# Optimization experiments

Hardware: AMD Instinct MI355X
Metric: run time of the kernel (lower is better)

## Reference

```python
import jax, jax.numpy as jnp
import numpy as np

B, T, L = 512, 512, 128  # batch, seq_len, tag-vocab size (incl. START=126, STOP=127)


def setup_inputs() -> dict:
    key = jax.random.key(0)
    k1, k2, k3 = jax.random.split(key, 3)
    # scale emissions so exp(gold path score) stays finite in fp32
    feats = jax.random.normal(k1, (B, T, L), dtype=jnp.float32) * 0.05
    # xavier_normal on [L, L] -> std = sqrt(2/(L+L)) = 1/sqrt(L)
    transfer = jax.random.normal(k2, (L, L), dtype=jnp.float32) * (1.0 / np.sqrt(L))
    target = jax.random.randint(k3, (B, T), 0, L - 2, dtype=jnp.int32)
    return {"feats": feats, "transfer": transfer, "target": target,
            "start": L - 2, "stop": L - 1}


def _crf_loss(feats, transfer, target, start, stop):
    # feats: [B, T, L] emissions; transfer: [L, L]; target: [B, T] gold tags
    Bb, Tt, Ll = feats.shape

    # ---- forward algorithm (log-sum-exp DP over tags) ----
    # scores[1] = feats[1] + transfer[start, :]
    prev0 = feats[:, 1] + transfer[start][None, :]  # [B, L]

    def step(prev, f_t):
        # original: scores[t, y] = LSE_x( scores[t-1, x] + feats[t, x] + transfer[x, y] )
        v = prev + f_t                                        # [B, L] over prev-tag x
        new = jax.nn.logsumexp(v[:, :, None] + transfer[None, :, :], axis=1)  # [B, L]
        return new, None

    step = jax.checkpoint(step)  # keep scan residuals to just the carries
    feats_rest = jnp.swapaxes(feats[:, 2:], 0, 1)  # [T-2, B, L]
    prev, _ = jax.lax.scan(step, prev0, feats_rest)
    sentence_score = jax.nn.logsumexp(prev + transfer[:, stop][None, :], axis=1)  # [B]

    # ---- gold path score ----
    emit0 = feats[:, 0, start]  # hh[0, start]
    emit = jnp.take_along_axis(feats[:, 1:], target[:, 1:, None], axis=2)[..., 0].sum(axis=1)
    pre = jnp.concatenate(
        [jnp.full((Bb, 1), start, dtype=target.dtype), target[:, 1:Tt - 1]], axis=1)  # [B, T-1]
    # original reads transfer[pre, tgt].data[0] -> detached constant
    trans = jax.lax.stop_gradient(transfer[pre, target[:, 1:]]).sum(axis=1)
    gold_score = jnp.exp(emit0 + emit + trans)  # original returns torch.exp(score)

    return sentence_score - gold_score  # per-sentence loss, shape [B]


def reference(feats, transfer, target, start, stop):
    return _crf_loss(feats, transfer, target, start, stop)
```

## Files before the change

kernel.cpp:

```cpp
#include <hip/hip_runtime.h>
#include <hip/hip_bf16.h>

#define T_DIM 512
#define L_DIM 128

typedef _Float16 h2 __attribute__((ext_vector_type(2)));

#if defined(__has_builtin)
#if __has_builtin(__builtin_amdgcn_fdot2)
#define HAS_FDOT2 1
#endif
#endif

__device__ __forceinline__ float fdot2_acc(h2 a, h2 b, float c) {
#ifdef HAS_FDOT2
    return __builtin_amdgcn_fdot2(a, b, c, false);
#else
    return c + (float)a.x * (float)b.x + (float)a.y * (float)b.y;
#endif
}

__device__ __forceinline__ h2 pack_f16(float a, float b) {
    return __builtin_bit_cast(h2, __builtin_amdgcn_cvt_pkrtz(a, b));
}

__device__ __forceinline__ void lds_barrier() {
    asm volatile("s_waitcnt lgkmcnt(0)\n\ts_barrier" ::: "memory");
}

__global__ __launch_bounds__(512, 4) void crf_fwd_kernel(
    const float* __restrict__ feats,
    const float* __restrict__ transfer,
    const int* __restrict__ target,
    const int* __restrict__ startp,
    const int* __restrict__ stopp,
    float* __restrict__ out)
{
    __shared__ unsigned short LdsU[2][L_DIM] __attribute__((aligned(16)));
    __shared__ float LdsRed[32];

    const int tid  = threadIdx.x;
    const int lane = tid & 63;
    const int wv   = tid >> 6;
    const int jj   = lane & 15;
    const int iq   = lane >> 4;
    const int j    = (wv << 4) | jj;
    const int i0   = iq << 5;
    const int b    = blockIdx.x;
    const int start = startp[0];
    const int stop  = stopp[0];
    const float* fbase = feats + (size_t)b * T_DIM * L_DIM;
    const float LOG128 = 4.852030263919617f;

    h2 Ecol[16];
#pragma unroll
    for (int q = 0; q < 16; ++q) {
        float e0 = __expf(transfer[(i0 + 2 * q)     * L_DIM + j]) * 0.0078125f;
        float e1 = __expf(transfer[(i0 + 2 * q + 1) * L_DIM + j]) * 0.0078125f;
        Ecol[q] = pack_f16(e0, e1);
    }
    const float trStop = transfer[j * L_DIM + stop];

    {
        float v2 = fbase[1 * L_DIM + j] + fbase[2 * L_DIM + j]
                 + transfer[start * L_DIM + j];
        if (iq == 0) {
            _Float16 h = (_Float16)__expf(v2);
            LdsU[0][j] = __builtin_bit_cast(unsigned short, h);
        }
    }
    float fa = fbase[3 * L_DIM + j];
    float fb = fbase[4 * L_DIM + j];
    float S  = 0.f;
    lds_barrier();

    int cur = 0;
    float accFinal = 0.f;

    for (int t = 2; t <= T_DIM - 1; ++t) {
        int tp = t + 3; if (tp > T_DIM - 1) tp = T_DIM - 1;
        float fnew = fbase[tp * L_DIM + j];
        float fexp = __expf(fa);

        if ((t & 15) == 0) {
            _Float16 h0 = __builtin_bit_cast(_Float16, LdsU[cur][0]);
            float u0 = (float)h0;
            fexp *= 1.0f / u0;
            S += __logf(u0);
        }

        const uint4* P4 = reinterpret_cast<const uint4*>(&LdsU[cur][0]);
        uint4 pa = P4[(iq << 2) | 0];
        uint4 pb = P4[(iq << 2) | 1];
        uint4 pc = P4[(iq << 2) | 2];
        uint4 pd = P4[(iq << 2) | 3];

        float a0 = 0.f, a1 = 0.f, a2 = 0.f, a3 = 0.f;
        a0 = fdot2_acc(__builtin_bit_cast(h2, pa.x), Ecol[0],  a0);
        a0 = fdot2_acc(__builtin_bit_cast(h2, pa.y), Ecol[1],  a0);
        a0 = fdot2_acc(__builtin_bit_cast(h2, pa.z), Ecol[2],  a0);
        a0 = fdot2_acc(__builtin_bit_cast(h2, pa.w), Ecol[3],  a0);
        a1 = fdot2_acc(__builtin_bit_cast(h2, pb.x), Ecol[4],  a1);
        a1 = fdot2_acc(__builtin_bit_cast(h2, pb.y), Ecol[5],  a1);
        a1 = fdot2_acc(__builtin_bit_cast(h2, pb.z), Ecol[6],  a1);
        a1 = fdot2_acc(__builtin_bit_cast(h2, pb.w), Ecol[7],  a1);
        a2 = fdot2_acc(__builtin_bit_cast(h2, pc.x), Ecol[8],  a2);
        a2 = fdot2_acc(__builtin_bit_cast(h2, pc.y), Ecol[9],  a2);
        a2 = fdot2_acc(__builtin_bit_cast(h2, pc.z), Ecol[10], a2);
        a2 = fdot2_acc(__builtin_bit_cast(h2, pc.w), Ecol[11], a2);
        a3 = fdot2_acc(__builtin_bit_cast(h2, pd.x), Ecol[12], a3);
        a3 = fdot2_acc(__builtin_bit_cast(h2, pd.y), Ecol[13], a3);
        a3 = fdot2_acc(__builtin_bit_cast(h2, pd.z), Ecol[14], a3);
        a3 = fdot2_acc(__builtin_bit_cast(h2, pd.w), Ecol[15], a3);
        float acc = (a0 + a1) + (a2 + a3);

        acc += __shfl_xor(acc, 16);
        acc += __shfl_xor(acc, 32);

        if (t < T_DIM - 1) {
            float un = acc * fexp;
            fa = fb; fb = fnew;
            if (iq == 0) {
                _Float16 h = (_Float16)un;
                LdsU[cur ^ 1][j] = __builtin_bit_cast(unsigned short, h);
            }
            lds_barrier();
            cur ^= 1;
        } else {
            accFinal = acc;
        }
    }

    S += 510.0f * LOG128;

    float x  = __logf(accFinal) + S + trStop;
    float mx = x;
#pragma unroll
    for (int d = 1; d < 64; d <<= 1) mx = fmaxf(mx, __shfl_xor(mx, d));
    float ex = (iq == 0) ? __expf(x - mx) : 0.f;
#pragma unroll
    for (int d = 1; d < 64; d <<= 1) ex += __shfl_xor(ex, d);
    if (lane == 0) { LdsRed[wv] = mx; LdsRed[8 + wv] = ex; }

    float es = 0.f, ts = 0.f;
    {
        int t = 1 + tid;
        if (t < T_DIM) {
            int tg = target[b * T_DIM + t];
            es = fbase[t * L_DIM + tg];
            int pr = (t == 1) ? start : target[b * T_DIM + t - 1];
            ts = transfer[pr * L_DIM + tg];
        }
    }
#pragma unroll
    for (int d = 1; d < 64; d <<= 1) {
        es += __shfl_xor(es, d);
        ts += __shfl_xor(ts, d);
    }
    if (lane == 0) { LdsRed[16 + wv] = es; LdsRed[24 + wv] = ts; }
    __syncthreads();

    if (tid == 0) {
        float M = LdsRed[0];
#pragma unroll
        for (int k = 1; k < 8; ++k) M = fmaxf(M, LdsRed[k]);
        float Ssum = 0.f;
#pragma unroll
        for (int k = 0; k < 8; ++k) Ssum += LdsRed[8 + k] * __expf(LdsRed[k] - M);
        float sentence = M + __logf(Ssum);
        float em = 0.f, tn = 0.f;
#pragma unroll
        for (int k = 0; k < 8; ++k) { em += LdsRed[16 + k]; tn += LdsRed[24 + k]; }
        float emit0 = fbase[start];
        out[b] = sentence - __expf(emit0 + em + tn);
    }
}

extern "C" void kernel_launch(void* const* d_in, const int* in_sizes, int n_in,
                              void* d_out, int out_size, void* d_ws, size_t ws_size,
                              hipStream_t stream) {
    const float* feats    = (const float*)d_in[0];
    const float* transfer = (const float*)d_in[1];
    const int*   target   = (const int*)d_in[2];
    const int*   startp   = (const int*)d_in[3];
    const int*   stopp    = (const int*)d_in[4];
    float* outp = (float*)d_out;
    int B = in_sizes[0] / (T_DIM * L_DIM);
    hipLaunchKernelGGL(crf_fwd_kernel, dim3(B), dim3(512), 0, stream,
                       feats, transfer, target, startp, stopp, outp);
}
```

Measured before the change: 396.3 us.

## Run each sequence's CRF recursion on a single wavefront without barriers

```diff
diff --git a/kernel.cpp b/kernel.cpp
--- a/kernel.cpp
+++ b/kernel.cpp
@@ -24,11 +24,11 @@
     return __builtin_bit_cast(h2, __builtin_amdgcn_cvt_pkrtz(a, b));
 }
 
-__device__ __forceinline__ void lds_barrier() {
-    asm volatile("s_waitcnt lgkmcnt(0)\n\ts_barrier" ::: "memory");
+__device__ __forceinline__ h2 uint_as_h2(unsigned int v) {
+    return __builtin_bit_cast(h2, v);
 }
 
-__global__ __launch_bounds__(512, 4) void crf_fwd_kernel(
+__global__ __launch_bounds__(64, 1) void crf_fwd_kernel(
     const float* __restrict__ feats,
     const float* __restrict__ transfer,
     const int* __restrict__ target,
@@ -36,120 +36,119 @@
     const int* __restrict__ stopp,
     float* __restrict__ out)
 {
-    __shared__ unsigned short LdsU[2][L_DIM] __attribute__((aligned(16)));
-    __shared__ float LdsRed[32];
+    __shared__ unsigned int LdsU[2][64] __attribute__((aligned(16)));
 
-    const int tid  = threadIdx.x;
-    const int lane = tid & 63;
-    const int wv   = tid >> 6;
-    const int jj   = lane & 15;
-    const int iq   = lane >> 4;
-    const int j    = (wv << 4) | jj;
-    const int i0   = iq << 5;
+    const int lane = threadIdx.x;
+    const int p    = lane;
+    const int j0   = p << 1;
+    const int j1   = j0 | 1;
     const int b    = blockIdx.x;
     const int start = startp[0];
     const int stop  = stopp[0];
     const float* fbase = feats + (size_t)b * T_DIM * L_DIM;
+    const float2* f2 = reinterpret_cast<const float2*>(fbase);
     const float LOG128 = 4.852030263919617f;
 
-    h2 Ecol[16];
+    h2 E0[64], E1[64];
 #pragma unroll
-    for (int q = 0; q < 16; ++q) {
-        float e0 = __expf(transfer[(i0 + 2 * q)     * L_DIM + j]) * 0.0078125f;
-        float e1 = __expf(transfer[(i0 + 2 * q + 1) * L_DIM + j]) * 0.0078125f;
-        Ecol[q] = pack_f16(e0, e1);
+    for (int q = 0; q < 64; ++q) {
+        const float2* r0 = reinterpret_cast<const float2*>(transfer + (2 * q) * L_DIM + j0);
+        const float2* r1 = reinterpret_cast<const float2*>(transfer + (2 * q + 1) * L_DIM + j0);
+        float2 e0 = *r0;
+        float2 e1 = *r1;
+        E0[q] = pack_f16(__expf(e0.x) * 0.0078125f, __expf(e1.x) * 0.0078125f);
+        E1[q] = pack_f16(__expf(e0.y) * 0.0078125f, __expf(e1.y) * 0.0078125f);
     }
-    const float trStop = transfer[j * L_DIM + stop];
+    const float trS0 = transfer[j0 * L_DIM + stop];
+    const float trS1 = transfer[j1 * L_DIM + stop];
 
     {
-        float v2 = fbase[1 * L_DIM + j] + fbase[2 * L_DIM + j]
-                 + transfer[start * L_DIM + j];
-        if (iq == 0) {
-            _Float16 h = (_Float16)__expf(v2);
-            LdsU[0][j] = __builtin_bit_cast(unsigned short, h);
-        }
+        float2 f1v = f2[1 * 64 + p];
+        float2 f2v = f2[2 * 64 + p];
+        const float2* ts = reinterpret_cast<const float2*>(transfer + start * L_DIM + j0);
+        float2 tsv = *ts;
+        float v0 = f1v.x + f2v.x + tsv.x;
+        float v1 = f1v.y + f2v.y + tsv.y;
+        LdsU[0][p] = __builtin_bit_cast(unsigned int, pack_f16(__expf(v0), __expf(v1)));
     }
-    float fa = fbase[3 * L_DIM + j];
-    float fb = fbase[4 * L_DIM + j];
-    float S  = 0.f;
-    lds_barrier();
+    float2 fa = f2[3 * 64 + p];
+    float2 fb = f2[4 * 64 + p];
+    float S = 0.f;
 
     int cur = 0;
-    float accFinal = 0.f;
+    float accF0 = 0.f, accF1 = 0.f;
 
     for (int t = 2; t <= T_DIM - 1; ++t) {
         int tp = t + 3; if (tp > T_DIM - 1) tp = T_DIM - 1;
-        float fnew = fbase[tp * L_DIM + j];
-        float fexp = __expf(fa);
+        float2 fnew = f2[tp * 64 + p];
+        float fe0 = __expf(fa.x);
+        float fe1 = __expf(fa.y);
+
+        asm volatile("s_waitcnt lgkmcnt(0)" ::: "memory");
+        const uint4* P4 = reinterpret_cast<const uint4*>(&LdsU[cur][0]);
+        uint4 R[16];
+#pragma unroll
+        for (int r = 0; r < 16; ++r) R[r] = P4[r];
 
         if ((t & 15) == 0) {
-            _Float16 h0 = __builtin_bit_cast(_Float16, LdsU[cur][0]);
-            float u0 = (float)h0;
-            fexp *= 1.0f / u0;
+            float u0 = (float)uint_as_h2(R[0].x).x;
+            float rr = __builtin_amdgcn_rcpf(u0);
             S += __logf(u0);
+            fe0 *= rr; fe1 *= rr;
         }
 
-        const uint4* P4 = reinterpret_cast<const uint4*>(&LdsU[cur][0]);
-        uint4 pa = P4[(iq << 2) | 0];
-        uint4 pb = P4[(iq << 2) | 1];
-        uint4 pc = P4[(iq << 2) | 2];
-        uint4 pd = P4[(iq << 2) | 3];
-
         float a0 = 0.f, a1 = 0.f, a2 = 0.f, a3 = 0.f;
-        a0 = fdot2_acc(__builtin_bit_cast(h2, pa.x), Ecol[0],  a0);
-        a0 = fdot2_acc(__builtin_bit_cast(h2, pa.y), Ecol[1],  a0);
-        a0 = fdot2_acc(__builtin_bit_cast(h2, pa.z), Ecol[2],  a0);
-        a0 = fdot2_acc(__builtin_bit_cast(h2, pa.w), Ecol[3],  a0);
-        a1 = fdot2_acc(__builtin_bit_cast(h2, pb.x), Ecol[4],  a1);
-        a1 = fdot2_acc(__builtin_bit_cast(h2, pb.y), Ecol[5],  a1);
-        a1 = fdot2_acc(__builtin_bit_cast(h2, pb.z), Ecol[6],  a1);
-        a1 = fdot2_acc(__builtin_bit_cast(h2, pb.w), Ecol[7],  a1);
-        a2 = fdot2_acc(__builtin_bit_cast(h2, pc.x), Ecol[8],  a2);
-        a2 = fdot2_acc(__builtin_bit_cast(h2, pc.y), Ecol[9],  a2);
-        a2 = fdot2_acc(__builtin_bit_cast(h2, pc.z), Ecol[10], a2);
-        a2 = fdot2_acc(__builtin_bit_cast(h2, pc.w), Ecol[11], a2);
-        a3 = fdot2_acc(__builtin_bit_cast(h2, pd.x), Ecol[12], a3);
-        a3 = fdot2_acc(__builtin_bit_cast(h2, pd.y), Ecol[13], a3);
-        a3 = fdot2_acc(__builtin_bit_cast(h2, pd.z), Ecol[14], a3);
-        a3 = fdot2_acc(__builtin_bit_cast(h2, pd.w), Ecol[15], a3);
-        float acc = (a0 + a1) + (a2 + a3);
-
-        acc += __shfl_xor(acc, 16);
-        acc += __shfl_xor(acc, 32);
+        float c0 = 0.f, c1 = 0.f, c2 = 0.f, c3 = 0.f;
+#pragma unroll
+        for (int r = 0; r < 16; ++r) {
+            h2 u0p = uint_as_h2(R[r].x);
+            h2 u1p = uint_as_h2(R[r].y);
+            h2 u2p = uint_as_h2(R[r].z);
+            h2 u3p = uint_as_h2(R[r].w);
+            a0 = fdot2_acc(u0p, E0[4 * r + 0], a0);
+            a1 = fdot2_acc(u1p, E0[4 * r + 1], a1);
+            a2 = fdot2_acc(u2p, E0[4 * r + 2], a2);
+            a3 = fdot2_acc(u3p, E0[4 * r + 3], a3);
+            c0 = fdot2_acc(u0p, E1[4 * r + 0], c0);
+            c1 = fdot2_acc(u1p, E1[4 * r + 1], c1);
+            c2 = fdot2_acc(u2p, E1[4 * r + 2], c2);
+            c3 = fdot2_acc(u3p, E1[4 * r + 3], c3);
+        }
+        float acc0 = (a0 + a1) + (a2 + a3);
+        float acc1 = (c0 + c1) + (c2 + c3);
 
         if (t < T_DIM - 1) {
-            float un = acc * fexp;
+            float un0 = acc0 * fe0;
+            float un1 = acc1 * fe1;
             fa = fb; fb = fnew;
-            if (iq == 0) {
-                _Float16 h = (_Float16)un;
-                LdsU[cur ^ 1][j] = __builtin_bit_cast(unsigned short, h);
-            }
-            lds_barrier();
+            LdsU[cur ^ 1][p] = __builtin_bit_cast(unsigned int, pack_f16(un0, un1));
             cur ^= 1;
         } else {
-            accFinal = acc;
+            accF0 = acc0; accF1 = acc1;
         }
     }
 
     S += 510.0f * LOG128;
 
-    float x  = __logf(accFinal) + S + trStop;
-    float mx = x;
+    float x0 = __logf(accF0) + S + trS0;
+    float x1 = __logf(accF1) + S + trS1;
+    float mx = fmaxf(x0, x1);
 #pragma unroll
     for (int d = 1; d < 64; d <<= 1) mx = fmaxf(mx, __shfl_xor(mx, d));
-    float ex = (iq == 0) ? __expf(x - mx) : 0.f;
+    float ex = __expf(x0 - mx) + __expf(x1 - mx);
 #pragma unroll
     for (int d = 1; d < 64; d <<= 1) ex += __shfl_xor(ex, d);
-    if (lane == 0) { LdsRed[wv] = mx; LdsRed[8 + wv] = ex; }
+    float sentence = mx + __logf(ex);
 
     float es = 0.f, ts = 0.f;
-    {
-        int t = 1 + tid;
+#pragma unroll
+    for (int k = 0; k < 8; ++k) {
+        int t = 1 + lane + (k << 6);
         if (t < T_DIM) {
             int tg = target[b * T_DIM + t];
-            es = fbase[t * L_DIM + tg];
+            es += fbase[t * L_DIM + tg];
             int pr = (t == 1) ? start : target[b * T_DIM + t - 1];
-            ts = transfer[pr * L_DIM + tg];
+            ts += transfer[pr * L_DIM + tg];
         }
     }
 #pragma unroll
@@ -157,22 +156,10 @@
         es += __shfl_xor(es, d);
         ts += __shfl_xor(ts, d);
     }
-    if (lane == 0) { LdsRed[16 + wv] = es; LdsRed[24 + wv] = ts; }
-    __syncthreads();
 
-    if (tid == 0) {
-        float M = LdsRed[0];
-#pragma unroll
-        for (int k = 1; k < 8; ++k) M = fmaxf(M, LdsRed[k]);
-        float Ssum = 0.f;
-#pragma unroll
-        for (int k = 0; k < 8; ++k) Ssum += LdsRed[8 + k] * __expf(LdsRed[k] - M);
-        float sentence = M + __logf(Ssum);
-        float em = 0.f, tn = 0.f;
-#pragma unroll
-        for (int k = 0; k < 8; ++k) { em += LdsRed[16 + k]; tn += LdsRed[24 + k]; }
+    if (lane == 0) {
         float emit0 = fbase[start];
-        out[b] = sentence - __expf(emit0 + em + tn);
+        out[b] = sentence - __expf(emit0 + es + ts);
     }
 }
 
@@ -186,6 +173,6 @@
     const int*   stopp    = (const int*)d_in[4];
     float* outp = (float*)d_out;
     int B = in_sizes[0] / (T_DIM * L_DIM);
-    hipLaunchKernelGGL(crf_fwd_kernel, dim3(B), dim3(512), 0, stream,
+    hipLaunchKernelGGL(crf_fwd_kernel, dim3(B), dim3(64), 0, stream,
                        feats, transfer, target, startp, stopp, outp);
 }
```

New measurement: 398.1 us. No clear change (+0.5%).
